# Performance work log

Measured on AMD Instinct MI355X. Metric: run time of the kernel, lower is better.

The kernel has to match this reference:

```python
import jax, jax.numpy as jnp
import numpy as np

TEMPERATURE = 0.07
N_ANCHORS = 256
THRESHOLD = 0.1
EPS_VALID = 1e-6


def setup_inputs() -> dict:
    key = jax.random.key(0)
    kf, kp, ka = jax.random.split(key, 3)
    B, N, D, H, W = 8, 4, 256, 48, 64
    HW = H * W
    # channels-first features, as the module's permute branch expects
    features = jax.random.normal(kf, (B, N, D, H, W), dtype=jnp.float32)
    # uniform[0,1) -> all points valid (norm > 1e-6) and NN dists mostly < threshold
    pointmaps = jax.random.uniform(kp, (B, N, H, W, 3), dtype=jnp.float32)
    # deterministic stand-in for torch.randperm(N_i)[:n_anchors], one per (view pair, batch)
    keys = jax.random.split(ka, (N - 1) * B)
    perm = jax.vmap(lambda k: jax.random.permutation(k, HW)[:N_ANCHORS])(keys)
    anchor_idx = perm.reshape(N - 1, B, N_ANCHORS).astype(jnp.int32)
    return {"features": features, "pointmaps": pointmaps, "anchor_idx": anchor_idx}


def _l2norm(x):
    # F.normalize(dim=-1) semantics
    return x / jnp.clip(jnp.linalg.norm(x, axis=-1, keepdims=True), 1e-12)


def _pair_loss(fi, fj, pi, pj, vi, vj, aidx):
    # fi, fj: [HW, D]; pi, pj: [HW, 3]; vi, vj: [HW] bool; aidx: [A]
    a_pts = pi[aidx]                                   # [A, 3]
    a_feats = fi[aidx]                                 # [A, D]
    # cdist(anchor_pts, pts_j): [A, HW]
    d2 = jnp.sum((a_pts[:, None, :] - pj[None, :, :]) ** 2, axis=-1)
    dists = jnp.sqrt(jnp.maximum(d2, 0.0))
    dists = jnp.where(vj[None, :], dists, jnp.inf)     # invalid j points can't be matched
    pos_idx = jnp.argmin(dists, axis=-1)               # [A]
    min_d = jnp.min(dists, axis=-1)                    # [A]
    valid_a = (min_d < THRESHOLD) & vi[aidx]           # anchor must be valid + matched
    a_n = _l2norm(a_feats)                             # [A, D]
    p_n = _l2norm(fj[pos_idx])                         # [A, D]
    all_n = _l2norm(fj)                                # [HW, D]
    pos_sim = jnp.sum(a_n * p_n, axis=-1) / TEMPERATURE            # [A]
    all_sim = jnp.einsum('ad,jd->aj', a_n, all_n) / TEMPERATURE    # [A, HW]
    all_sim = jnp.where(vj[None, :], all_sim, -jnp.inf)            # mask invalid negatives
    loss_a = -pos_sim + jax.nn.logsumexp(all_sim, axis=-1)         # [A]
    cnt = jnp.sum(valid_a)
    loss_b = jnp.sum(jnp.where(valid_a, loss_a, 0.0)) / jnp.maximum(cnt, 1)
    include = (cnt >= 5) & (jnp.sum(vi) >= 10) & (jnp.sum(vj) >= 10)
    return loss_b, include


def reference(features, pointmaps, anchor_idx):
    if features.shape[-1] != features.shape[-2]:
        features = jnp.transpose(features, (0, 1, 3, 4, 2))  # [B,N,D,H,W] -> [B,N,H,W,D]
    B, N, H, W, D = features.shape
    feats = features.reshape(B, N, H * W, D)
    pts = pointmaps.reshape(B, N, H * W, 3)
    valid = jnp.linalg.norm(pts, axis=-1) > EPS_VALID    # [B, N, HW]
    total = jnp.float32(0.0)
    for v in range(1, N):  # small fixed loop over view pairs (0, v)
        lb, inc = jax.vmap(_pair_loss)(
            feats[:, 0], feats[:, v], pts[:, 0], pts[:, v],
            valid[:, 0], valid[:, v], anchor_idx[v - 1])
        n_inc = jnp.sum(inc)
        pair = jnp.where(n_inc > 0,
                         jnp.sum(jnp.where(inc, lb, 0.0)) / jnp.maximum(n_inc, 1),
                         0.0)
        total = total + pair
    return total / max(N - 1, 1)
```

## Files before the change

kernel.cpp:

```cpp
#include <hip/hip_runtime.h>
#include <math.h>

#define B_ 8
#define N_ 4
#define D_ 256
#define HW_ 3072
#define A_ 256
#define NP_ 3
#define NJT2_ 48
#define NJB_ 48
#define INV_T 14.2857142857142857f
#define LDKH 64

typedef _Float16 half8 __attribute__((ext_vector_type(8)));
typedef _Float16 half2v __attribute__((ext_vector_type(2)));
typedef float f32x4 __attribute__((ext_vector_type(4)));

__global__ __launch_bounds__(256) void k_prep(const float* __restrict__ f,
        const float* __restrict__ pts, _Float16* __restrict__ fh,
        unsigned char* __restrict__ valid, int* __restrict__ vcnt_part) {
  __shared__ unsigned tile[4][64 * 32];
  __shared__ float ssql[4][16][4];
  __shared__ float srn[64];
  int j0 = blockIdx.x * 64;
  int bn = blockIdx.y;
  int n = bn & 3;
  int tid = threadIdx.x;
  int jq = tid & 15;
  int dr = tid >> 4;

  float ssq0 = 0.f, ssq1 = 0.f, ssq2 = 0.f, ssq3 = 0.f;
#pragma unroll
  for (int dt = 0; dt < 4; ++dt) {
    const float* fb = f + ((size_t)bn * D_ + dt * 64 + 4 * dr) * HW_ + j0 + 4 * jq;
    f32x4 r0 = *(const f32x4*)&fb[0];
    f32x4 r1 = *(const f32x4*)&fb[HW_];
    f32x4 r2 = *(const f32x4*)&fb[2 * HW_];
    f32x4 r3 = *(const f32x4*)&fb[3 * HW_];
    ssq0 = fmaf(r0[0], r0[0], fmaf(r1[0], r1[0], fmaf(r2[0], r2[0], fmaf(r3[0], r3[0], ssq0))));
    ssq1 = fmaf(r0[1], r0[1], fmaf(r1[1], r1[1], fmaf(r2[1], r2[1], fmaf(r3[1], r3[1], ssq1))));
    ssq2 = fmaf(r0[2], r0[2], fmaf(r1[2], r1[2], fmaf(r2[2], r2[2], fmaf(r3[2], r3[2], ssq2))));
    ssq3 = fmaf(r0[3], r0[3], fmaf(r1[3], r1[3], fmaf(r2[3], r2[3], fmaf(r3[3], r3[3], ssq3))));
    int p0 = 2 * dr;
#pragma unroll
    for (int jj = 0; jj < 4; ++jj) {
      int jl = 4 * jq + jj;
      half2v h01, h23;
      h01[0] = (_Float16)r0[jj]; h01[1] = (_Float16)r1[jj];
      h23[0] = (_Float16)r2[jj]; h23[1] = (_Float16)r3[jj];
      tile[dt][jl * 32 + (p0 ^ (jl & 31))]       = __builtin_bit_cast(unsigned, h01);
      tile[dt][jl * 32 + ((p0 + 1) ^ (jl & 31))] = __builtin_bit_cast(unsigned, h23);
    }
  }
  ssq0 += __shfl_xor(ssq0, 16); ssq0 += __shfl_xor(ssq0, 32);
  ssq1 += __shfl_xor(ssq1, 16); ssq1 += __shfl_xor(ssq1, 32);
  ssq2 += __shfl_xor(ssq2, 16); ssq2 += __shfl_xor(ssq2, 32);
  ssq3 += __shfl_xor(ssq3, 16); ssq3 += __shfl_xor(ssq3, 32);
  if ((tid & 63) < 16) {
    int w = tid >> 6;
    ssql[w][jq][0] = ssq0; ssql[w][jq][1] = ssq1;
    ssql[w][jq][2] = ssq2; ssql[w][jq][3] = ssq3;
  }
  __syncthreads();
  if (tid < 64) {
    float s = ssql[0][tid >> 2][tid & 3] + ssql[1][tid >> 2][tid & 3]
            + ssql[2][tid >> 2][tid & 3] + ssql[3][tid >> 2][tid & 3];
    float r = 1.f / fmaxf(sqrtf(s), 1e-12f);
    srn[tid] = (n == 0) ? r * INV_T : r;
    size_t idx = (size_t)bn * HW_ + j0 + tid;
    const float* p = pts + idx * 3;
    float x = p[0], y = p[1], z = p[2];
    int v = (x * x + y * y + z * z) > 1e-12f ? 1 : 0;
    valid[idx] = (unsigned char)v;
    unsigned long long mask = __ballot(v);
    if (tid == 0) vcnt_part[bn * NJB_ + blockIdx.x] = __popcll(mask);
  }
  __syncthreads();
  unsigned* outw = (unsigned*)fh;
  int c = tid & 31;
  int jr = tid >> 5;
#pragma unroll
  for (int dt = 0; dt < 4; ++dt) {
#pragma unroll
    for (int pass = 0; pass < 8; ++pass) {
      int j = jr + pass * 8;
      float sc = srn[j];
      unsigned u = tile[dt][j * 32 + (c ^ (j & 31))];
      half2v h = __builtin_bit_cast(half2v, u);
      half2v o;
      o[0] = (_Float16)((float)h[0] * sc);
      o[1] = (_Float16)((float)h[1] * sc);
      outw[((size_t)bn * HW_ + j0 + j) * (D_ / 2) + dt * 32 + c] =
          __builtin_bit_cast(unsigned, o);
    }
  }
}

__global__ __launch_bounds__(256) void k_nn(const float* __restrict__ pts,
    const int* __restrict__ aidx, int* __restrict__ pos_idx,
    unsigned char* __restrict__ valid_a, int* __restrict__ ticket) {
  if (blockIdx.x == 0 && threadIdx.x == 0) *ticket = 0;
  int wave = threadIdx.x >> 6, lane = threadIdx.x & 63;
  int gid = blockIdx.x;
  int agrp = gid & 63;
  int b = (gid >> 6) & 7;
  int p = gid >> 9;
  int a = agrp * 4 + wave;
  int vv = p + 1;
  int col = aidx[(p * B_ + b) * A_ + a];
  const float* pi = pts + ((size_t)(b * N_) * HW_ + col) * 3;
  float ax = pi[0], ay = pi[1], az = pi[2];
  int vi = (ax * ax + ay * ay + az * az) > 1e-12f ? 1 : 0;
  const f32x4* pj4 = (const f32x4*)(pts + (size_t)(b * N_ + vv) * HW_ * 3);
  float best = INFINITY; int bidx = 0x7fffffff;
#pragma unroll 2
  for (int t = 0; t < HW_ / 256; ++t) {
    int jb = t * 256 + lane * 4;
    int base = t * 192 + lane * 3;
    f32x4 q0 = pj4[base + 0];
    f32x4 q1 = pj4[base + 1];
    f32x4 q2 = pj4[base + 2];
    float px[4] = {q0[0], q0[3], q1[2], q2[1]};
    float py[4] = {q0[1], q1[0], q1[3], q2[2]};
    float pz[4] = {q0[2], q1[1], q2[0], q2[3]};
#pragma unroll
    for (int k = 0; k < 4; ++k) {
      float x = px[k], y = py[k], z = pz[k];
      int vj = (x * x + y * y + z * z) > 1e-12f;
      float dx = ax - x, dy = ay - y, dz = az - z;
      float dist = sqrtf(dx * dx + dy * dy + dz * dz);
      int j = jb + k;
      if (vj && (dist < best || (dist == best && j < bidx))) { best = dist; bidx = j; }
    }
  }
#pragma unroll
  for (int o = 32; o > 0; o >>= 1) {
    float ob = __shfl_xor(best, o);
    int oi = __shfl_xor(bidx, o);
    if (ob < best || (ob == best && oi < bidx)) { best = ob; bidx = oi; }
  }
  if (lane == 0) {
    int ai = (p * B_ + b) * A_ + a;
    pos_idx[ai] = (bidx == 0x7fffffff) ? 0 : bidx;
    valid_a[ai] = (best < 0.1f) && vi;
  }
}

#define STAGE_AB(KK, BUF) do {                                                 \
  _Pragma("unroll")                                                            \
  for (int cc = 0; cc < 4; ++cc) {                                             \
    const _Float16* srcA = fA + (size_t)colA[cc] * D_ + (KK) * 64 + gsw * 8;   \
    __builtin_amdgcn_global_load_lds(                                          \
        (const __attribute__((address_space(1))) void*)srcA,                   \
        (__attribute__((address_space(3))) void*)&As[BUF][(wid * 32 + cc * 8) * LDKH], \
        16, 0, 0);                                                             \
  }                                                                            \
  _Pragma("unroll")                                                            \
  for (int cc = 0; cc < 4; ++cc) {                                             \
    const _Float16* srcB = fB + (size_t)rowB[cc] * D_ + (KK) * 64 + gsw * 8;   \
    __builtin_amdgcn_global_load_lds(                                          \
        (const __attribute__((address_space(1))) void*)srcB,                   \
        (__attribute__((address_space(3))) void*)&Bs[BUF][(wid * 32 + cc * 8) * LDKH], \
        16, 0, 0);                                                             \
  }                                                                            \
} while (0)

__global__ __launch_bounds__(256) void k_gemm(const _Float16* __restrict__ fh,
    const int* __restrict__ aidx, const unsigned char* __restrict__ valid,
    const int* __restrict__ pos_idx, float* __restrict__ possim,
    float2* __restrict__ partials) {
  __shared__ __align__(16) _Float16 As[2][128 * LDKH];
  __shared__ __align__(16) _Float16 Bs[2][128 * LDKH];
  int jt = blockIdx.x;
  int pbm = blockIdx.y;
  int pb = pbm >> 1, mt = pbm & 1;
  int b = pb & 7, p = pb >> 3, v = p + 1;
  int tid = threadIdx.x;
  int wid = tid >> 6, lane = tid & 63;
  int wr = wid >> 1, wc = wid & 1;
  int j0 = jt * 128;
  const _Float16* fA = fh + (size_t)(b * N_) * HW_ * D_;
  const _Float16* fB = fh + (size_t)(b * N_ + v) * HW_ * D_;

  int rl = lane >> 3;
  int gl = lane & 7;
  int gsw = gl ^ rl;
  int colA[4];
#pragma unroll
  for (int c = 0; c < 4; ++c)
    colA[c] = aidx[(p * B_ + b) * A_ + mt * 128 + wid * 32 + c * 8 + rl];
  int rowB[4];
#pragma unroll
  for (int c = 0; c < 4; ++c) rowB[c] = j0 + wid * 32 + c * 8 + rl;

  f32x4 acc[4][4];
#pragma unroll
  for (int m = 0; m < 4; ++m)
#pragma unroll
    for (int n = 0; n < 4; ++n) acc[m][n] = (f32x4)0.f;

  int kg = lane >> 4;
  int fr = lane & 15;

  STAGE_AB(0, 0);
  __syncthreads();

#pragma unroll
  for (int kk = 0; kk < 4; ++kk) {
    const int cur = kk & 1;
    if (kk < 3) STAGE_AB(kk + 1, cur ^ 1);
#pragma unroll
    for (int s = 0; s < 2; ++s) {
      half8 af[4], bf[4];
      int G = s * 4 + kg;
#pragma unroll
      for (int m = 0; m < 4; ++m) {
        int row = wr * 64 + m * 16 + fr;
        af[m] = *(half8*)&As[cur][row * LDKH + ((G ^ (row & 7)) << 3)];
      }
#pragma unroll
      for (int n = 0; n < 4; ++n) {
        int row = wc * 64 + n * 16 + fr;
        bf[n] = *(half8*)&Bs[cur][row * LDKH + ((G ^ (row & 7)) << 3)];
      }
      __builtin_amdgcn_s_setprio(1);
#pragma unroll
      for (int m = 0; m < 4; ++m)
#pragma unroll
        for (int n = 0; n < 4; ++n)
          acc[m][n] = __builtin_amdgcn_mfma_f32_16x16x32_f16(af[m], bf[n], acc[m][n], 0, 0, 0);
      __builtin_amdgcn_s_setprio(0);
    }
    if (kk < 3) __syncthreads();
  }

  int jb = j0 + wc * 64;
  int vrow = b * N_ + v;
  int vm[4]; int jn[4];
#pragma unroll
  for (int n = 0; n < 4; ++n) {
    jn[n] = jb + n * 16 + fr;
    vm[n] = valid[(size_t)vrow * HW_ + jn[n]];
  }
#pragma unroll
  for (int m = 0; m < 4; ++m) {
    int abase = mt * 128 + wr * 64 + m * 16 + kg * 4;
#pragma unroll
    for (int reg = 0; reg < 4; ++reg) {
      int a = abase + reg;
      int ai = pb * A_ + a;
      int pidx = pos_idx[ai];
      float sv[4]; float mx = -INFINITY;
#pragma unroll
      for (int n = 0; n < 4; ++n) {
        sv[n] = acc[m][n][reg];
        if (vm[n]) mx = fmaxf(mx, sv[n]);
      }
#pragma unroll
      for (int n = 0; n < 4; ++n)
        if (jn[n] == pidx) possim[ai] = sv[n];
#pragma unroll
      for (int o = 1; o < 16; o <<= 1) mx = fmaxf(mx, __shfl_xor(mx, o));
      float S = 0.f;
#pragma unroll
      for (int n = 0; n < 4; ++n)
        if (vm[n]) S += __expf(sv[n] - mx);
#pragma unroll
      for (int o = 1; o < 16; o <<= 1) S += __shfl_xor(S, o);
      if (fr == 0) partials[(size_t)ai * NJT2_ + (jt * 2 + wc)] = make_float2(mx, S);
    }
  }
}

__global__ __launch_bounds__(1024) void k_merge(const float2* __restrict__ partials,
    const float* __restrict__ possim, const unsigned char* __restrict__ valid_a,
    const int* __restrict__ vcnt_part, float* __restrict__ lossb,
    int* __restrict__ incb, int* __restrict__ ticket, float* __restrict__ out) {
  int pb = blockIdx.x;
  int b = pb & 7, p = pb >> 3;
  int tid = threadIdx.x;
  int a = tid >> 2, q = tid & 3;
  int ai = pb * A_ + a;

  __shared__ float ss[16]; __shared__ int sc[16];
  __shared__ int v0c, vvc;
  if (tid == 0) { v0c = 0; vvc = 0; }
  __syncthreads();
  if (tid < NJB_) atomicAdd(&v0c, vcnt_part[(b * N_ + 0) * NJB_ + tid]);
  else if (tid < 2 * NJB_) atomicAdd(&vvc, vcnt_part[(b * N_ + p + 1) * NJB_ + (tid - NJB_)]);

  const float4* pt = (const float4*)partials + (size_t)ai * 24 + q * 6;
  float4 vv4[6];
#pragma unroll
  for (int i = 0; i < 6; ++i) vv4[i] = pt[i];
  float mx = -INFINITY;
#pragma unroll
  for (int i = 0; i < 6; ++i) { mx = fmaxf(mx, vv4[i].x); mx = fmaxf(mx, vv4[i].z); }
  float S = 0.f;
  if (mx != -INFINITY) {
#pragma unroll
    for (int i = 0; i < 6; ++i) {
      S += vv4[i].y * __expf(vv4[i].x - mx);
      S += vv4[i].w * __expf(vv4[i].z - mx);
    }
  }
  float am = mx;
#pragma unroll
  for (int o = 1; o < 4; o <<= 1) am = fmaxf(am, __shfl_xor(am, o));
  float Sg = S * ((mx == am) ? 1.f : __expf(mx - am));
#pragma unroll
  for (int o = 1; o < 4; o <<= 1) Sg += __shfl_xor(Sg, o);

  float contrib = 0.f; int cnt = 0;
  if (q == 0) {
    float lse = (am == -INFINITY) ? -INFINITY : am + logf(Sg);
    if (valid_a[ai]) { contrib = lse - possim[ai]; cnt = 1; }
  }
#pragma unroll
  for (int o = 4; o < 64; o <<= 1) {
    contrib += __shfl_xor(contrib, o);
    cnt += __shfl_xor(cnt, o);
  }
  if ((tid & 63) == 0) { ss[tid >> 6] = contrib; sc[tid >> 6] = cnt; }
  __syncthreads();
  if (tid == 0) {
    float s = 0.f; int c = 0;
#pragma unroll
    for (int i = 0; i < 16; ++i) { s += ss[i]; c += sc[i]; }
    float lb = s / (float)(c > 1 ? c : 1);
    int inc = (c >= 5) && (v0c >= 10) && (vvc >= 10);
    lossb[pb] = lb;
    incb[pb] = inc;
    __threadfence();
    int old = atomicAdd(ticket, 1);
    if (old == NP_ * B_ - 1) {
      __threadfence();
      float total = 0.f;
      for (int pp = 0; pp < NP_; ++pp) {
        float sacc = 0.f; int n = 0;
        for (int bb = 0; bb < B_; ++bb)
          if (incb[pp * B_ + bb]) { sacc += lossb[pp * B_ + bb]; ++n; }
        total += (n > 0) ? sacc / (float)n : 0.f;
      }
      out[0] = total / (float)NP_;
    }
  }
}

extern "C" void kernel_launch(void* const* d_in, const int* in_sizes, int n_in,
                              void* d_out, int out_size, void* d_ws, size_t ws_size,
                              hipStream_t stream) {
  const float* f   = (const float*)d_in[0];
  const float* pts = (const float*)d_in[1];
  const int* aidx  = (const int*)d_in[2];
  float* out = (float*)d_out;

  char* ws = (char*)d_ws;
  _Float16* fh          = (_Float16*)(ws);
  unsigned char* valid  = (unsigned char*)(ws + 50331648);
  int* pos_idx          = (int*)(ws + 50429952);
  unsigned char* valid_a= (unsigned char*)(ws + 50454528);
  float* possim         = (float*)(ws + 50460672);
  float* lossb          = (float*)(ws + 50485248);
  int* incb             = (int*)(ws + 50485376);
  float2* partials      = (float2*)(ws + 50485504);
  int* vcnt_part        = (int*)(ws + 52844800);
  int* ticket           = (int*)(ws + 52850944);

  k_prep<<<dim3(HW_ / 64, B_ * N_), 256, 0, stream>>>(f, pts, fh, valid, vcnt_part);
  k_nn<<<NP_ * B_ * (A_ / 4), 256, 0, stream>>>(pts, aidx, pos_idx, valid_a, ticket);
  k_gemm<<<dim3(24, NP_ * B_ * 2), 256, 0, stream>>>(fh, aidx, valid, pos_idx, possim, partials);
  k_merge<<<NP_ * B_, 1024, 0, stream>>>(partials, possim, valid_a, vcnt_part, lossb, incb, ticket, out);
}
```

Measured before the change: 104.5 us.

## Stage GEMM accumulators through LDS for per-thread row softmax partials

```diff
diff --git a/kernel.cpp b/kernel.cpp
--- a/kernel.cpp
+++ b/kernel.cpp
@@ -169,8 +169,11 @@
     const int* __restrict__ aidx, const unsigned char* __restrict__ valid,
     const int* __restrict__ pos_idx, float* __restrict__ possim,
     float2* __restrict__ partials) {
-  __shared__ __align__(16) _Float16 As[2][128 * LDKH];
-  __shared__ __align__(16) _Float16 Bs[2][128 * LDKH];
+  __shared__ __align__(16) char smem[65536];
+  _Float16 (*As)[128 * LDKH] = reinterpret_cast<_Float16 (*)[128 * LDKH]>(smem);
+  _Float16 (*Bs)[128 * LDKH] = reinterpret_cast<_Float16 (*)[128 * LDKH]>(smem + 32768);
+  float (*scr)[132] = reinterpret_cast<float (*)[132]>(smem);
+
   int jt = blockIdx.x;
   int pbm = blockIdx.y;
   int pb = pbm >> 1, mt = pbm & 1;
@@ -234,41 +237,47 @@
     if (kk < 3) __syncthreads();
   }
 
-  int jb = j0 + wc * 64;
+  __syncthreads();
+
   int vrow = b * N_ + v;
-  int vm[4]; int jn[4];
-#pragma unroll
-  for (int n = 0; n < 4; ++n) {
-    jn[n] = jb + n * 16 + fr;
-    vm[n] = valid[(size_t)vrow * HW_ + jn[n]];
-  }
-#pragma unroll
-  for (int m = 0; m < 4; ++m) {
-    int abase = mt * 128 + wr * 64 + m * 16 + kg * 4;
-#pragma unroll
-    for (int reg = 0; reg < 4; ++reg) {
-      int a = abase + reg;
-      int ai = pb * A_ + a;
-      int pidx = pos_idx[ai];
-      float sv[4]; float mx = -INFINITY;
-#pragma unroll
-      for (int n = 0; n < 4; ++n) {
-        sv[n] = acc[m][n][reg];
-        if (vm[n]) mx = fmaxf(mx, sv[n]);
-      }
-#pragma unroll
-      for (int n = 0; n < 4; ++n)
-        if (jn[n] == pidx) possim[ai] = sv[n];
-#pragma unroll
-      for (int o = 1; o < 16; o <<= 1) mx = fmaxf(mx, __shfl_xor(mx, o));
-      float S = 0.f;
-#pragma unroll
-      for (int n = 0; n < 4; ++n)
-        if (vm[n]) S += __expf(sv[n] - mx);
-#pragma unroll
-      for (int o = 1; o < 16; o <<= 1) S += __shfl_xor(S, o);
-      if (fr == 0) partials[(size_t)ai * NJT2_ + (jt * 2 + wc)] = make_float2(mx, S);
-    }
+  int a_loc = tid >> 1, h = tid & 1;
+  int aig = pb * A_ + mt * 128 + a_loc;
+  int pidx = pos_idx[aig];
+
+#pragma unroll
+  for (int pss = 0; pss < 2; ++pss) {
+    if (wc == pss) {
+#pragma unroll
+      for (int m = 0; m < 4; ++m)
+#pragma unroll
+        for (int n = 0; n < 4; ++n)
+          *(f32x4*)&scr[n * 16 + fr][wr * 64 + m * 16 + kg * 4] = acc[m][n];
+    }
+    __syncthreads();
+    int jbase = j0 + pss * 64 + h * 32;
+    const unsigned* vp = (const unsigned*)(valid + (size_t)vrow * HW_ + jbase);
+    unsigned vw[8];
+#pragma unroll
+    for (int w = 0; w < 8; ++w) vw[w] = vp[w];
+    float vv[32];
+#pragma unroll
+    for (int jj = 0; jj < 32; ++jj) vv[jj] = scr[h * 32 + jj][a_loc];
+    float mx = -INFINITY;
+#pragma unroll
+    for (int jj = 0; jj < 32; ++jj) {
+      if ((vw[jj >> 2] >> ((jj & 3) * 8)) & 0xff) mx = fmaxf(mx, vv[jj]);
+      if (jbase + jj == pidx) possim[aig] = vv[jj];
+    }
+    float S = 0.f;
+#pragma unroll
+    for (int jj = 0; jj < 32; ++jj) {
+      if ((vw[jj >> 2] >> ((jj & 3) * 8)) & 0xff) S += __expf(vv[jj] - mx);
+    }
+    float am = fmaxf(mx, __shfl_xor(mx, 1));
+    float Ss = (mx == am) ? S : S * __expf(mx - am);
+    Ss += __shfl_xor(Ss, 1);
+    if (h == 0) partials[(size_t)aig * NJT2_ + (jt * 2 + pss)] = make_float2(am, Ss);
+    __syncthreads();
   }
 }
 
```

New measurement: 90.30 us. 1.16x faster.

## Restructure similarity GEMM to keep anchor features in registers with online logsumexp

Applied to the files above, without the earlier changes.

```diff
diff --git a/kernel.cpp b/kernel.cpp
--- a/kernel.cpp
+++ b/kernel.cpp
@@ -7,10 +7,11 @@
 #define HW_ 3072
 #define A_ 256
 #define NP_ 3
-#define NJT2_ 48
 #define NJB_ 48
 #define INV_T 14.2857142857142857f
-#define LDKH 64
+#define JC_ 32
+#define JSP_ 96
+#define PSL_ 32
 
 typedef _Float16 half8 __attribute__((ext_vector_type(8)));
 typedef _Float16 half2v __attribute__((ext_vector_type(2)));
@@ -146,178 +147,194 @@
   }
 }
 
-#define STAGE_AB(KK, BUF) do {                                                 \
+#define STAGE_B(CH, BB) do {                                                   \
   _Pragma("unroll")                                                            \
-  for (int cc = 0; cc < 4; ++cc) {                                             \
-    const _Float16* srcA = fA + (size_t)colA[cc] * D_ + (KK) * 64 + gsw * 8;   \
+  for (int c = 0; c < 2; ++c) {                                                \
+    int rw = wid * 4 + c * 2 + r2;                                             \
+    const _Float16* src = fB + (size_t)(jB + (CH) * 32 + rw) * D_              \
+                          + ((gs ^ (rw & 31)) << 3);                           \
     __builtin_amdgcn_global_load_lds(                                          \
-        (const __attribute__((address_space(1))) void*)srcA,                   \
-        (__attribute__((address_space(3))) void*)&As[BUF][(wid * 32 + cc * 8) * LDKH], \
-        16, 0, 0);                                                             \
-  }                                                                            \
-  _Pragma("unroll")                                                            \
-  for (int cc = 0; cc < 4; ++cc) {                                             \
-    const _Float16* srcB = fB + (size_t)rowB[cc] * D_ + (KK) * 64 + gsw * 8;   \
-    __builtin_amdgcn_global_load_lds(                                          \
-        (const __attribute__((address_space(1))) void*)srcB,                   \
-        (__attribute__((address_space(3))) void*)&Bs[BUF][(wid * 32 + cc * 8) * LDKH], \
+        (const __attribute__((address_space(1))) void*)src,                    \
+        (__attribute__((address_space(3))) void*)&Bl[BB][(wid * 4 + c * 2) * 256], \
         16, 0, 0);                                                             \
   }                                                                            \
 } while (0)
 
-__global__ __launch_bounds__(256) void k_gemm(const _Float16* __restrict__ fh,
+__global__ __launch_bounds__(512, 4) void k_gemm(const _Float16* __restrict__ fh,
     const int* __restrict__ aidx, const unsigned char* __restrict__ valid,
     const int* __restrict__ pos_idx, float* __restrict__ possim,
     float2* __restrict__ partials) {
-  __shared__ __align__(16) _Float16 As[2][128 * LDKH];
-  __shared__ __align__(16) _Float16 Bs[2][128 * LDKH];
+  __shared__ __align__(16) _Float16 Bl[2][32 * 256];
   int jt = blockIdx.x;
-  int pbm = blockIdx.y;
-  int pb = pbm >> 1, mt = pbm & 1;
+  int pb = blockIdx.y;
   int b = pb & 7, p = pb >> 3, v = p + 1;
   int tid = threadIdx.x;
   int wid = tid >> 6, lane = tid & 63;
-  int wr = wid >> 1, wc = wid & 1;
-  int j0 = jt * 128;
+  int kg = lane >> 4, fr = lane & 15;
+  int jB = jt * JSP_;
   const _Float16* fA = fh + (size_t)(b * N_) * HW_ * D_;
   const _Float16* fB = fh + (size_t)(b * N_ + v) * HW_ * D_;
-
-  int rl = lane >> 3;
-  int gl = lane & 7;
-  int gsw = gl ^ rl;
-  int colA[4];
-#pragma unroll
-  for (int c = 0; c < 4; ++c)
-    colA[c] = aidx[(p * B_ + b) * A_ + mt * 128 + wid * 32 + c * 8 + rl];
-  int rowB[4];
-#pragma unroll
-  for (int c = 0; c < 4; ++c) rowB[c] = j0 + wid * 32 + c * 8 + rl;
-
-  f32x4 acc[4][4];
-#pragma unroll
-  for (int m = 0; m < 4; ++m)
-#pragma unroll
-    for (int n = 0; n < 4; ++n) acc[m][n] = (f32x4)0.f;
-
-  int kg = lane >> 4;
-  int fr = lane & 15;
-
-  STAGE_AB(0, 0);
-  __syncthreads();
-
-#pragma unroll
-  for (int kk = 0; kk < 4; ++kk) {
-    const int cur = kk & 1;
-    if (kk < 3) STAGE_AB(kk + 1, cur ^ 1);
-#pragma unroll
-    for (int s = 0; s < 2; ++s) {
-      half8 af[4], bf[4];
-      int G = s * 4 + kg;
-#pragma unroll
-      for (int m = 0; m < 4; ++m) {
-        int row = wr * 64 + m * 16 + fr;
-        af[m] = *(half8*)&As[cur][row * LDKH + ((G ^ (row & 7)) << 3)];
-      }
-#pragma unroll
-      for (int n = 0; n < 4; ++n) {
-        int row = wc * 64 + n * 16 + fr;
-        bf[n] = *(half8*)&Bs[cur][row * LDKH + ((G ^ (row & 7)) << 3)];
-      }
-      __builtin_amdgcn_s_setprio(1);
-#pragma unroll
-      for (int m = 0; m < 4; ++m)
-#pragma unroll
-        for (int n = 0; n < 4; ++n)
-          acc[m][n] = __builtin_amdgcn_mfma_f32_16x16x32_f16(af[m], bf[n], acc[m][n], 0, 0, 0);
-      __builtin_amdgcn_s_setprio(0);
-    }
-    if (kk < 3) __syncthreads();
-  }
-
-  int jb = j0 + wc * 64;
   int vrow = b * N_ + v;
-  int vm[4]; int jn[4];
-#pragma unroll
-  for (int n = 0; n < 4; ++n) {
-    jn[n] = jb + n * 16 + fr;
-    vm[n] = valid[(size_t)vrow * HW_ + jn[n]];
-  }
-#pragma unroll
-  for (int m = 0; m < 4; ++m) {
-    int abase = mt * 128 + wr * 64 + m * 16 + kg * 4;
-#pragma unroll
-    for (int reg = 0; reg < 4; ++reg) {
-      int a = abase + reg;
-      int ai = pb * A_ + a;
-      int pidx = pos_idx[ai];
-      float sv[4]; float mx = -INFINITY;
-#pragma unroll
-      for (int n = 0; n < 4; ++n) {
-        sv[n] = acc[m][n][reg];
-        if (vm[n]) mx = fmaxf(mx, sv[n]);
-      }
-#pragma unroll
-      for (int n = 0; n < 4; ++n)
-        if (jn[n] == pidx) possim[ai] = sv[n];
-#pragma unroll
-      for (int o = 1; o < 16; o <<= 1) mx = fmaxf(mx, __shfl_xor(mx, o));
-      float S = 0.f;
-#pragma unroll
-      for (int n = 0; n < 4; ++n)
-        if (vm[n]) S += __expf(sv[n] - mx);
-#pragma unroll
-      for (int o = 1; o < 16; o <<= 1) S += __shfl_xor(S, o);
-      if (fr == 0) partials[(size_t)ai * NJT2_ + (jt * 2 + wc)] = make_float2(mx, S);
-    }
-  }
-}
-
-__global__ __launch_bounds__(1024) void k_merge(const float2* __restrict__ partials,
+
+  int abase = pb * A_ + wid * 32;
+  int col0 = aidx[abase + fr];
+  int col1 = aidx[abase + 16 + fr];
+  half8 af0[8], af1[8];
+#pragma unroll
+  for (int ks = 0; ks < 8; ++ks) {
+    af0[ks] = *(const half8*)&fA[(size_t)col0 * D_ + ks * 32 + kg * 8];
+    af1[ks] = *(const half8*)&fA[(size_t)col1 * D_ + ks * 32 + kg * 8];
+  }
+  int pidx0 = pos_idx[abase + fr];
+  int pidx1 = pos_idx[abase + 16 + fr];
+
+  int r2 = lane >> 5, gs = lane & 31;
+
+  float m0 = -INFINITY, S0 = 0.f, ps0 = 0.f, fn0 = 0.f;
+  float m1 = -INFINITY, S1 = 0.f, ps1 = 0.f, fn1 = 0.f;
+
+  STAGE_B(0, 0);
+  __syncthreads();
+
+#pragma unroll
+  for (int ch = 0; ch < 3; ++ch) {
+    const int cur = ch & 1;
+    if (ch < 2) STAGE_B(ch + 1, cur ^ 1);
+    f32x4 acc00 = (f32x4)0.f, acc01 = (f32x4)0.f;
+    f32x4 acc10 = (f32x4)0.f, acc11 = (f32x4)0.f;
+#pragma unroll
+    for (int ks = 0; ks < 8; ++ks) {
+      int g = ks * 4 + kg;
+      int rb0 = fr;
+      int rb1 = 16 + fr;
+      half8 bf0 = *(half8*)&Bl[cur][rb0 * 256 + ((g ^ (rb0 & 31)) << 3)];
+      half8 bf1 = *(half8*)&Bl[cur][rb1 * 256 + ((g ^ (rb1 & 31)) << 3)];
+      acc00 = __builtin_amdgcn_mfma_f32_16x16x32_f16(bf0, af0[ks], acc00, 0, 0, 0);
+      acc01 = __builtin_amdgcn_mfma_f32_16x16x32_f16(bf1, af0[ks], acc01, 0, 0, 0);
+      acc10 = __builtin_amdgcn_mfma_f32_16x16x32_f16(bf0, af1[ks], acc10, 0, 0, 0);
+      acc11 = __builtin_amdgcn_mfma_f32_16x16x32_f16(bf1, af1[ks], acc11, 0, 0, 0);
+    }
+    int jb0 = jB + ch * 32;
+    unsigned vw0 = *(const unsigned*)(valid + (size_t)vrow * HW_ + jb0 + kg * 4);
+    unsigned vw1 = *(const unsigned*)(valid + (size_t)vrow * HW_ + jb0 + 16 + kg * 4);
+    {
+      float cm = -INFINITY;
+#pragma unroll
+      for (int r = 0; r < 4; ++r) {
+        if ((vw0 >> (r * 8)) & 0xff) cm = fmaxf(cm, acc00[r]);
+        if ((vw1 >> (r * 8)) & 0xff) cm = fmaxf(cm, acc01[r]);
+      }
+      if (cm != -INFINITY) {
+        float nm = fmaxf(m0, cm);
+        S0 *= __expf(m0 - nm);
+#pragma unroll
+        for (int r = 0; r < 4; ++r) {
+          if ((vw0 >> (r * 8)) & 0xff) S0 += __expf(acc00[r] - nm);
+          if ((vw1 >> (r * 8)) & 0xff) S0 += __expf(acc01[r] - nm);
+        }
+        m0 = nm;
+      }
+#pragma unroll
+      for (int r = 0; r < 4; ++r) {
+        if (jb0 + kg * 4 + r == pidx0)      { ps0 = acc00[r]; fn0 = 1.f; }
+        if (jb0 + 16 + kg * 4 + r == pidx0) { ps0 = acc01[r]; fn0 = 1.f; }
+      }
+    }
+    {
+      float cm = -INFINITY;
+#pragma unroll
+      for (int r = 0; r < 4; ++r) {
+        if ((vw0 >> (r * 8)) & 0xff) cm = fmaxf(cm, acc10[r]);
+        if ((vw1 >> (r * 8)) & 0xff) cm = fmaxf(cm, acc11[r]);
+      }
+      if (cm != -INFINITY) {
+        float nm = fmaxf(m1, cm);
+        S1 *= __expf(m1 - nm);
+#pragma unroll
+        for (int r = 0; r < 4; ++r) {
+          if ((vw0 >> (r * 8)) & 0xff) S1 += __expf(acc10[r] - nm);
+          if ((vw1 >> (r * 8)) & 0xff) S1 += __expf(acc11[r] - nm);
+        }
+        m1 = nm;
+      }
+#pragma unroll
+      for (int r = 0; r < 4; ++r) {
+        if (jb0 + kg * 4 + r == pidx1)      { ps1 = acc10[r]; fn1 = 1.f; }
+        if (jb0 + 16 + kg * 4 + r == pidx1) { ps1 = acc11[r]; fn1 = 1.f; }
+      }
+    }
+    if (ch < 2) __syncthreads();
+  }
+
+#pragma unroll
+  for (int o = 16; o <= 32; o <<= 1) {
+    {
+      float om = __shfl_xor(m0, o), oS = __shfl_xor(S0, o);
+      float nm = fmaxf(m0, om);
+      S0 = ((m0 == nm) ? S0 : S0 * __expf(m0 - nm))
+         + ((om == nm) ? oS : oS * __expf(om - nm));
+      m0 = nm;
+    }
+    {
+      float om = __shfl_xor(m1, o), oS = __shfl_xor(S1, o);
+      float nm = fmaxf(m1, om);
+      S1 = ((m1 == nm) ? S1 : S1 * __expf(m1 - nm))
+         + ((om == nm) ? oS : oS * __expf(om - nm));
+      m1 = nm;
+    }
+    ps0 += __shfl_xor(ps0, o); fn0 += __shfl_xor(fn0, o);
+    ps1 += __shfl_xor(ps1, o); fn1 += __shfl_xor(fn1, o);
+  }
+  if (kg == 0) {
+    int aig0 = abase + fr;
+    int aig1 = abase + 16 + fr;
+    partials[(size_t)aig0 * PSL_ + jt] = make_float2(m0, S0);
+    partials[(size_t)aig1 * PSL_ + jt] = make_float2(m1, S1);
+    if (fn0 > 0.5f) possim[aig0] = ps0;
+    if (fn1 > 0.5f) possim[aig1] = ps1;
+  }
+}
+
+__global__ __launch_bounds__(256) void k_merge(const float2* __restrict__ partials,
     const float* __restrict__ possim, const unsigned char* __restrict__ valid_a,
     const int* __restrict__ vcnt_part, float* __restrict__ lossb,
     int* __restrict__ incb, int* __restrict__ ticket, float* __restrict__ out) {
   int pb = blockIdx.x;
   int b = pb & 7, p = pb >> 3;
   int tid = threadIdx.x;
-  int a = tid >> 2, q = tid & 3;
-  int ai = pb * A_ + a;
-
-  __shared__ float ss[16]; __shared__ int sc[16];
+  int ai = pb * A_ + tid;
+
+  __shared__ float ss[4]; __shared__ int sc[4];
   __shared__ int v0c, vvc;
   if (tid == 0) { v0c = 0; vvc = 0; }
   __syncthreads();
   if (tid < NJB_) atomicAdd(&v0c, vcnt_part[(b * N_ + 0) * NJB_ + tid]);
-  else if (tid < 2 * NJB_) atomicAdd(&vvc, vcnt_part[(b * N_ + p + 1) * NJB_ + (tid - NJB_)]);
-
-  const float4* pt = (const float4*)partials + (size_t)ai * 24 + q * 6;
-  float4 vv4[6];
-#pragma unroll
-  for (int i = 0; i < 6; ++i) vv4[i] = pt[i];
+  else if (tid >= 128 && tid < 128 + NJB_)
+    atomicAdd(&vvc, vcnt_part[(b * N_ + p + 1) * NJB_ + (tid - 128)]);
+
+  const float4* pt = (const float4*)partials + (size_t)ai * (PSL_ / 2);
+  float4 vv4[16];
+#pragma unroll
+  for (int i = 0; i < 16; ++i) vv4[i] = pt[i];
   float mx = -INFINITY;
 #pragma unroll
-  for (int i = 0; i < 6; ++i) { mx = fmaxf(mx, vv4[i].x); mx = fmaxf(mx, vv4[i].z); }
+  for (int i = 0; i < 16; ++i) { mx = fmaxf(mx, vv4[i].x); mx = fmaxf(mx, vv4[i].z); }
   float S = 0.f;
   if (mx != -INFINITY) {
 #pragma unroll
-    for (int i = 0; i < 6; ++i) {
+    for (int i = 0; i < 16; ++i) {
       S += vv4[i].y * __expf(vv4[i].x - mx);
       S += vv4[i].w * __expf(vv4[i].z - mx);
     }
   }
-  float am = mx;
-#pragma unroll
-  for (int o = 1; o < 4; o <<= 1) am = fmaxf(am, __shfl_xor(am, o));
-  float Sg = S * ((mx == am) ? 1.f : __expf(mx - am));
-#pragma unroll
-  for (int o = 1; o < 4; o <<= 1) Sg += __shfl_xor(Sg, o);
-
   float contrib = 0.f; int cnt = 0;
-  if (q == 0) {
-    float lse = (am == -INFINITY) ? -INFINITY : am + logf(Sg);
-    if (valid_a[ai]) { contrib = lse - possim[ai]; cnt = 1; }
-  }
-#pragma unroll
-  for (int o = 4; o < 64; o <<= 1) {
+  if (valid_a[ai]) {
+    float lse = (mx == -INFINITY) ? -INFINITY : mx + logf(S);
+    contrib = lse - possim[ai];
+    cnt = 1;
+  }
+#pragma unroll
+  for (int o = 1; o < 64; o <<= 1) {
     contrib += __shfl_xor(contrib, o);
     cnt += __shfl_xor(cnt, o);
   }
@@ -326,7 +343,7 @@
   if (tid == 0) {
     float s = 0.f; int c = 0;
 #pragma unroll
-    for (int i = 0; i < 16; ++i) { s += ss[i]; c += sc[i]; }
+    for (int i = 0; i < 4; ++i) { s += ss[i]; c += sc[i]; }
     float lb = s / (float)(c > 1 ? c : 1);
     int inc = (c >= 5) && (v0c >= 10) && (vvc >= 10);
     lossb[pb] = lb;
@@ -369,6 +386,6 @@
 
   k_prep<<<dim3(HW_ / 64, B_ * N_), 256, 0, stream>>>(f, pts, fh, valid, vcnt_part);
   k_nn<<<NP_ * B_ * (A_ / 4), 256, 0, stream>>>(pts, aidx, pos_idx, valid_a, ticket);
-  k_gemm<<<dim3(24, NP_ * B_ * 2), 256, 0, stream>>>(fh, aidx, valid, pos_idx, possim, partials);
-  k_merge<<<NP_ * B_, 1024, 0, stream>>>(partials, possim, valid_a, vcnt_part, lossb, incb, ticket, out);
-}
+  k_gemm<<<dim3(JC_, NP_ * B_), 512, 0, stream>>>(fh, aidx, valid, pos_idx, possim, partials);
+  k_merge<<<NP_ * B_, 256, 0, stream>>>(partials, possim, valid_a, vcnt_part, lossb, incb, ticket, out);
+}
```

Measured after the change: 111.6 us. 6.8% more time.
